# Performance work log

Hardware: AMD Instinct MI355X
Metric: run time of the kernel (lower is better)

## Reference

```python
import jax, jax.numpy as jnp
import numpy as np
from math import factorial

# ---- static config mirroring Cace.__init__ ----
MAX_L = 3            # max angular degree
N_RBF = 8            # Bessel radial basis size
RB = 8               # n_radial_basis (radial embedding dim after transform)
K = 3                # n_atom_basis -> edge channels C = K*K
NZ = 4               # len(zs)
CUTOFF = 5.5
N_NODES = 2000
N_EDGES = 50000
T_MP = 1             # num_message_passing
MP_NORM = 1.0 / np.sqrt(25.0)   # 1/sqrt(avg_num_neighbors)
C = K * K

def _lxlylz(max_l):
    out = []
    for l in range(max_l + 1):
        for lx in range(l, -1, -1):
            for ly in range(l - lx, -1, -1):
                out.append((lx, ly, l - lx - ly))
    return out

L_LIST = _lxlylz(MAX_L)                 # 20 Cartesian monomials for max_l=3
NL = len(L_LIST)
LX = np.array([t[0] for t in L_LIST]); LY = np.array([t[1] for t in L_LIST]); LZ = np.array([t[2] for t in L_LIST])
DEGS = LX + LY + LZ                     # degree l of each monomial
MULTI = np.array([factorial(int(d)) / (factorial(int(a)) * factorial(int(b)) * factorial(int(c)))
                  for a, b, c, d in zip(LX, LY, LZ, DEGS)], dtype=np.float32)
SEL = np.zeros((NL, MAX_L + 1), np.float32)
SEL[np.arange(NL), DEGS] = 1.0          # monomial -> degree one-hot (for per-l sums)
NB = 1 + (MAX_L + 1)                    # symmetrizer feats: nu=1 (l=0) + nu=2 per l

def bessel(r):  # [E] -> [E, N_RBF]
    n = jnp.arange(1, N_RBF + 1, dtype=r.dtype)
    return jnp.sqrt(2.0 / CUTOFF) * jnp.sin(n[None, :] * jnp.pi * r[:, None] / CUTOFF) / r[:, None]

def poly_cutoff(r):  # MACE-style polynomial cutoff, p=6
    p = 6.0
    u = r / CUTOFF
    f = 1.0 - (p + 1.0) * (p + 2.0) / 2.0 * u**6 + p * (p + 2.0) * u**7 - p * (p + 1.0) / 2.0 * u**8
    return f * (u < 1.0)

def axis_pows(x):  # [E] -> [E, MAX_L+1] = x^0..x^MAX_L (safe grads, handles negatives)
    pows = [jnp.ones_like(x)]
    for _ in range(MAX_L):
        pows.append(pows[-1] * x)
    return jnp.stack(pows, axis=1)

def angular(u):  # unit vectors [E,3] -> Cartesian monomials [E, NL]
    return axis_pows(u[:, 0])[:, LX] * axis_pows(u[:, 1])[:, LY] * axis_pows(u[:, 2])[:, LZ]

def radial_transform(x, W):  # x [N,R,L,C], W [MAX_L+1,R,Rb] shared per degree l
    return jnp.einsum('nrlc,lrb->nblc', x, W[DEGS])

def symmetrize(A):  # A [N,Rb,NL,C] -> B [N,Rb,NB,C]
    b1 = A[:, :, :1, :]  # nu=1: the (0,0,0) monomial (index 0)
    w = (A * A) * jnp.asarray(MULTI)[None, None, :, None]
    b2 = jnp.einsum('nrlc,lm->nrmc', w, jnp.asarray(SEL))  # nu=2 invariant per degree l
    return jnp.concatenate([b1, b2], axis=2)


def setup_inputs() -> dict:
    key = jax.random.key(0)
    ks = jax.random.split(key, 9)
    positions = jax.random.uniform(ks[0], (N_NODES, 3), dtype=jnp.float32) * 12.0
    species = jax.random.randint(ks[1], (N_NODES,), 0, NZ)
    send = jax.random.randint(ks[2], (N_EDGES,), 0, N_NODES)
    off = jax.random.randint(ks[3], (N_EDGES,), 1, N_NODES)
    recv = (send + off) % N_NODES  # no self-edges -> strictly positive edge lengths
    edge_index = jnp.stack([send, recv])
    shifts = jnp.zeros((N_EDGES, 3), jnp.float32)
    W_embed = jax.random.normal(ks[4], (NZ, K), jnp.float32)
    W_radial = jax.random.normal(ks[5], (MAX_L + 1, N_RBF, RB), jnp.float32) / np.sqrt(N_RBF)
    W_mem = jax.random.normal(ks[6], (MAX_L + 1, RB, RB), jnp.float32) / np.sqrt(RB)
    W_ar = jax.random.normal(ks[7], (N_RBF, RB), jnp.float32) / np.sqrt(N_RBF)
    W_chi = jax.random.normal(ks[8], (RB, NB), jnp.float32) * 0.1
    return {"positions": positions, "shifts": shifts, "W_embed": W_embed, "W_radial": W_radial,
            "W_mem": W_mem, "W_ar": W_ar, "W_chi": W_chi, "species": species, "edge_index": edge_index}


def reference(positions, shifts, W_embed, W_radial, W_mem, W_ar, W_chi, species, edge_index):
    n_nodes = positions.shape[0]
    send, recv = edge_index[0], edge_index[1]
    # edge geometry
    vec = positions[recv] - positions[send] + shifts
    lengths = jnp.linalg.norm(vec, axis=-1)
    u = vec / (lengths[:, None] + 1e-9)
    rad = bessel(lengths)          # [E,R]
    fcut = poly_cutoff(lengths)    # [E]
    ang = angular(u)               # [E,NL]
    # edge type encoding: outer product of sender/receiver species embeddings
    emb = W_embed[species]         # [N,K]
    enc = (emb[send][:, :, None] * emb[recv][:, None, :]).reshape(-1, C)  # [E,C]
    # elementwise_multiply_3tensors -> [E,R,NL,C]
    edge_attri = jnp.einsum('er,el,ec->erlc', rad * fcut[:, None], ang, enc)
    A = radial_transform(jax.ops.segment_sum(edge_attri, recv, num_segments=n_nodes), W_radial)  # [N,Rb,NL,C]
    B = symmetrize(A)              # [N,Rb,NB,C]
    feats = [B]
    for _ in range(T_MP):
        mem = jnp.einsum('nrlc,lrb->nblc', A, W_mem[DEGS])        # NodeMemory
        chi = jnp.einsum('nbkc,bk->nc', B, W_chi)                  # MessageBchi node scalar
        msg_bchi = edge_attri * chi[send][:, None, None, :]
        A_bchi = radial_transform(jax.ops.segment_sum(msg_bchi, recv, num_segments=n_nodes), W_radial)
        fr = (rad @ W_ar) * fcut[:, None]                          # MessageAr radial filter [E,Rb]
        msg_ar = A[send] * fr[:, :, None, None]
        A_ar = jax.ops.segment_sum(msg_ar, recv, num_segments=n_nodes)
        A = (A_ar + A_bchi) * MP_NORM + mem
        B = symmetrize(A)
        feats.append(B)
    return jnp.stack(feats, axis=-1)   # [N,Rb,NB,C,T_MP+1]
```

## Files before the change

### kernel.cpp

```cpp
#include <hip/hip_runtime.h>
#include <hip/hip_bf16.h>


#define CUTF 5.5f
#define MPNORM 0.2f

__constant__ int   d_DEGS[20]  = {0,1,1,1,2,2,2,2,2,2,3,3,3,3,3,3,3,3,3,3};
__constant__ float d_MULTI[20] = {1,1,1,1,1,2,2,1,2,1,1,3,3,3,6,3,1,3,3,1};

__global__ void k_count(const int* __restrict__ eidx, int* __restrict__ counts, int E) {
  int e = blockIdx.x * blockDim.x + threadIdx.x;
  if (e < E) atomicAdd(&counts[eidx[E + e]], 1);
}

__global__ void k_scan(const int* __restrict__ counts, int* __restrict__ offs, int N) {
  __shared__ int part[256];
  int t = threadIdx.x;
  int local[8]; int sum = 0;
  #pragma unroll
  for (int i = 0; i < 8; i++) {
    int idx = t*8 + i;
    int v = (idx < N) ? counts[idx] : 0;
    local[i] = sum; sum += v;
  }
  part[t] = sum; __syncthreads();
  for (int d = 1; d < 256; d <<= 1) {
    int add = (t >= d) ? part[t-d] : 0;
    __syncthreads();
    part[t] += add;
    __syncthreads();
  }
  int excl = part[t] - sum;
  #pragma unroll
  for (int i = 0; i < 8; i++) {
    int idx = t*8 + i;
    if (idx < N) offs[idx] = excl + local[i];
  }
  if (t == 255) offs[N] = part[255];
}

__global__ void k_edge(const float* __restrict__ pos,
                       const float* __restrict__ shifts,
                       const float* __restrict__ Wemb,
                       const float* __restrict__ War,
                       const int* __restrict__ species,
                       const int* __restrict__ eidx,
                       const int* __restrict__ offs,
                       int* __restrict__ cursor,
                       float* __restrict__ edata,
                       int* __restrict__ esend,
                       int E) {
  __shared__ float war_s[64];
  int t = threadIdx.x;
  if (t < 64) war_s[t] = War[t];
  __syncthreads();
  int e = blockIdx.x * blockDim.x + t;
  if (e >= E) return;
  int s  = eidx[e];
  int rI = eidx[E + e];
  float vx = pos[rI*3+0] - pos[s*3+0] + shifts[e*3+0];
  float vy = pos[rI*3+1] - pos[s*3+1] + shifts[e*3+1];
  float vz = pos[rI*3+2] - pos[s*3+2] + shifts[e*3+2];
  float len = sqrtf(vx*vx + vy*vy + vz*vz);
  float inv = 1.0f / (len + 1e-9f);
  float ux = vx*inv, uy = vy*inv, uz = vz*inv;
  float uu = len * (1.0f/CUTF);
  float u2 = uu*uu, u6 = u2*u2*u2;
  float fcut = (uu < 1.0f) ? (1.0f - 28.0f*u6 + 48.0f*u6*uu - 21.0f*u6*u2) : 0.0f;
  float x = 3.14159265358979f * uu;
  float sn = sinf(x), c2 = 2.0f*cosf(x), snm1 = 0.0f;
  float pref = sqrtf(2.0f/CUTF) / (len + 1e-20f);
  float rad[8];
  float v[48];
  #pragma unroll
  for (int k = 0; k < 8; k++) {
    rad[k] = pref * sn;
    v[k]   = rad[k] * fcut;
    float nxt = c2*sn - snm1; snm1 = sn; sn = nxt;
  }
  #pragma unroll
  for (int b = 0; b < 8; b++) {
    float a = 0.0f;
    #pragma unroll
    for (int k = 0; k < 8; k++) a += rad[k] * war_s[k*8+b];
    v[8+b] = a * fcut;
  }
  float px2 = ux*ux, py2 = uy*uy, pz2 = uz*uz;
  v[16] = 1.0f; v[17] = ux;     v[18] = uy;     v[19] = uz;
  v[20] = px2;  v[21] = ux*uy;  v[22] = ux*uz;  v[23] = py2;
  v[24] = uy*uz;v[25] = pz2;
  v[26] = px2*ux; v[27] = px2*uy; v[28] = px2*uz; v[29] = ux*py2;
  v[30] = ux*uy*uz; v[31] = ux*pz2; v[32] = py2*uy; v[33] = py2*uz;
  v[34] = uy*pz2; v[35] = pz2*uz;
  int zs = species[s], zr = species[rI];
  float es0 = Wemb[zs*3+0], es1 = Wemb[zs*3+1], es2 = Wemb[zs*3+2];
  float er0 = Wemb[zr*3+0], er1 = Wemb[zr*3+1], er2 = Wemb[zr*3+2];
  v[36] = es0*er0; v[37] = es0*er1; v[38] = es0*er2;
  v[39] = es1*er0; v[40] = es1*er1; v[41] = es1*er2;
  v[42] = es2*er0; v[43] = es2*er1; v[44] = es2*er2;
  v[45] = 0.0f; v[46] = 0.0f; v[47] = 0.0f;
  int slot = atomicAdd(&cursor[rI], 1);
  int dst = offs[rI] + slot;
  float4* eb4 = reinterpret_cast<float4*>(edata + (size_t)dst * 48);
  #pragma unroll
  for (int w = 0; w < 12; w++)
    eb4[w] = make_float4(v[4*w], v[4*w+1], v[4*w+2], v[4*w+3]);
  esend[dst] = s;
}

__global__ __launch_bounds__(192) void k_nodeA(
    const float* __restrict__ edata, const int* __restrict__ offs,
    const float* __restrict__ Wrad, const float* __restrict__ Wchi,
    float* __restrict__ A, unsigned int* __restrict__ Abf2,
    float* __restrict__ chi, float* __restrict__ B0, int N) {
  __shared__ float wr_s[288];
  __shared__ float wchi_s[40];
  __shared__ float Bsh[360];
  int t = threadIdx.x, n = blockIdx.x;
  for (int i = t; i < 256; i += 192) { int d = i >> 6, rm = i & 63; wr_s[d*72+rm] = Wrad[i]; }
  for (int i = t; i < 40;  i += 192) wchi_s[i] = Wchi[i];
  for (int i = t; i < 360; i += 192) Bsh[i] = 0.0f;
  int l = t / 9, c = t - l*9;
  bool act = t < 180;
  int ll = act ? l : 0, cc = act ? c : 0;
  float acc[8];
  #pragma unroll
  for (int r = 0; r < 8; r++) acc[r] = 0.0f;
  int start = offs[n], end = offs[n+1];
  #pragma unroll 4
  for (int j = start; j < end; j++) {
    const float* row = edata + (size_t)j * 48;
    float p = row[16+ll] * row[36+cc];
    #pragma unroll
    for (int r = 0; r < 8; r++) acc[r] += row[r] * p;
  }
  __syncthreads();
  int deg = act ? d_DEGS[ll] : 0;
  const float* wp = &wr_s[deg*72];
  float Ab[8];
  #pragma unroll
  for (int b = 0; b < 8; b++) {
    float a = 0.0f;
    #pragma unroll
    for (int r = 0; r < 8; r++) a += acc[r] * wp[r*8+b];
    Ab[b] = a;
  }
  if (act) {
    #pragma unroll
    for (int b = 0; b < 8; b++) A[(size_t)n*1440 + t*8 + b] = Ab[b];
    #pragma unroll
    for (int bp = 0; bp < 4; bp++) {
      __hip_bfloat16 blo = __float2bfloat16(Ab[2*bp]);
      __hip_bfloat16 bhi = __float2bfloat16(Ab[2*bp+1]);
      unsigned int pr = (unsigned int)(*reinterpret_cast<unsigned short*>(&blo))
                      | ((unsigned int)(*reinterpret_cast<unsigned short*>(&bhi)) << 16);
      Abf2[(size_t)bp*N*180 + (size_t)n*180 + t] = pr;
    }
    if (l == 0) {
      #pragma unroll
      for (int b = 0; b < 8; b++) Bsh[b*45 + c] = Ab[b];
    }
    float mlt = d_MULTI[ll]; int kk = 1 + deg;
    #pragma unroll
    for (int b = 0; b < 8; b++) atomicAdd(&Bsh[b*45 + kk*9 + c], mlt*Ab[b]*Ab[b]);
  }
  __syncthreads();
  if (t < 9) {
    float s = 0.0f;
    for (int b = 0; b < 8; b++)
      #pragma unroll
      for (int kq = 0; kq < 5; kq++) s += Bsh[b*45 + kq*9 + t] * wchi_s[b*5 + kq];
    chi[n*9 + t] = s;
  }
  for (int i = t; i < 360; i += 192)
    B0[(size_t)n*360 + i] = Bsh[i];
}

__global__ __launch_bounds__(192) void k_node2(
    const float* __restrict__ edata, const int* __restrict__ esend,
    const int* __restrict__ offs,
    const float* __restrict__ Wrad, const float* __restrict__ Wmem,
    const float* __restrict__ A, const unsigned int* __restrict__ Abf2,
    const float* __restrict__ chi, const float* __restrict__ B0,
    float* __restrict__ out, int N) {
  __shared__ float wr_s[288], wm_s[288];
  __shared__ float Bsh[360];
  int t = threadIdx.x, n = blockIdx.x;
  for (int i = t; i < 256; i += 192) {
    int d = i >> 6, rm = i & 63;
    wr_s[d*72+rm] = Wrad[i];
    wm_s[d*72+rm] = Wmem[i];
  }
  for (int i = t; i < 360; i += 192) Bsh[i] = 0.0f;
  int l = t / 9, c = t - l*9;
  bool act = t < 180;
  int ll = act ? l : 0, cc = act ? c : 0;
  int tt = act ? t : 0;
  size_t plane = (size_t)N * 180;
  float Sacc[8], ARacc[8];
  #pragma unroll
  for (int r = 0; r < 8; r++) { Sacc[r] = 0.0f; ARacc[r] = 0.0f; }
  int start = offs[n], end = offs[n+1];
  #pragma unroll 4
  for (int j = start; j < end; j++) {
    const float* row = edata + (size_t)j * 48;
    int snd = esend[j];
    float ch = chi[snd*9 + cc];
    float pch = row[16+ll] * row[36+cc] * ch;
    #pragma unroll
    for (int r = 0; r < 8; r++) Sacc[r] += row[r] * pch;
    const unsigned int* gp = Abf2 + (size_t)snd*180 + tt;
    unsigned int q0 = gp[0];
    unsigned int q1 = gp[plane];
    unsigned int q2 = gp[2*plane];
    unsigned int q3 = gp[3*plane];
    float a0 = __uint_as_float(q0 << 16), a1 = __uint_as_float(q0 & 0xffff0000u);
    float a2 = __uint_as_float(q1 << 16), a3 = __uint_as_float(q1 & 0xffff0000u);
    float a4 = __uint_as_float(q2 << 16), a5 = __uint_as_float(q2 & 0xffff0000u);
    float a6 = __uint_as_float(q3 << 16), a7 = __uint_as_float(q3 & 0xffff0000u);
    ARacc[0] += a0*row[8];  ARacc[1] += a1*row[9];
    ARacc[2] += a2*row[10]; ARacc[3] += a3*row[11];
    ARacc[4] += a4*row[12]; ARacc[5] += a5*row[13];
    ARacc[6] += a6*row[14]; ARacc[7] += a7*row[15];
  }
  __syncthreads();
  if (act) {
    int deg = d_DEGS[ll];
    const float* wrp = &wr_s[deg*72];
    const float* wmp = &wm_s[deg*72];
    const float* aop = A + (size_t)n*1440 + t*8;
    float aown[8];
    #pragma unroll
    for (int r = 0; r < 8; r++) aown[r] = aop[r];
    float newA[8];
    #pragma unroll
    for (int b = 0; b < 8; b++) {
      float mem = 0.0f, ab = 0.0f;
      #pragma unroll
      for (int r = 0; r < 8; r++) { mem += aown[r]*wmp[r*8+b]; ab += Sacc[r]*wrp[r*8+b]; }
      newA[b] = (ARacc[b] + ab)*MPNORM + mem;
    }
    if (l == 0) {
      #pragma unroll
      for (int b = 0; b < 8; b++) Bsh[b*45 + c] = newA[b];
    }
    float mlt = d_MULTI[ll]; int kk = 1 + deg;
    #pragma unroll
    for (int b = 0; b < 8; b++) atomicAdd(&Bsh[b*45 + kk*9 + c], mlt*newA[b]*newA[b]);
  }
  __syncthreads();
  float2* out2 = reinterpret_cast<float2*>(out);
  for (int i = t; i < 360; i += 192) {
    float2 pk; pk.x = B0[(size_t)n*360 + i]; pk.y = Bsh[i];
    out2[(size_t)n*360 + i] = pk;
  }
}

extern "C" void kernel_launch(void* const* d_in, const int* in_sizes, int n_in,
                              void* d_out, int out_size, void* d_ws, size_t ws_size,
                              hipStream_t stream) {
  const float* pos    = (const float*)d_in[0];
  const float* shifts = (const float*)d_in[1];
  const float* Wemb   = (const float*)d_in[2];
  const float* Wrad   = (const float*)d_in[3];
  const float* Wmem   = (const float*)d_in[4];
  const float* War    = (const float*)d_in[5];
  const float* Wchi   = (const float*)d_in[6];
  const int* species = (const int*)d_in[7];
  const int* eidx    = (const int*)d_in[8];
  float* out = (float*)d_out;
  int N = in_sizes[7];
  int E = in_sizes[8] / 2;

  char* base = (char*)d_ws;
  size_t off = 0;
  float* edata = (float*)(base + off); off += (size_t)E*48*4;
  float* A     = (float*)(base + off); off += (size_t)N*1440*4;
  unsigned int* Abf2 = (unsigned int*)(base + off); off += (size_t)N*180*4*4;
  float* chi   = (float*)(base + off); off += (size_t)N*9*4;
  float* B0    = (float*)(base + off); off += (size_t)N*360*4;
  int* counts  = (int*)(base + off);   off += (size_t)N*4;
  int* cursor  = (int*)(base + off);   off += (size_t)N*4;
  int* offs    = (int*)(base + off);   off += (((size_t)(N+1)*4) + 15) & ~(size_t)15;
  int* esend   = (int*)(base + off);   off += (size_t)E*4;

  hipMemsetAsync(counts, 0, (size_t)N*2*4, stream);
  int eb = (E + 255) / 256;
  k_count<<<eb, 256, 0, stream>>>(eidx, counts, E);
  k_scan<<<1, 256, 0, stream>>>(counts, offs, N);
  k_edge<<<eb, 256, 0, stream>>>(pos, shifts, Wemb, War, species, eidx, offs, cursor,
                                 edata, esend, E);
  k_nodeA<<<N, 192, 0, stream>>>(edata, offs, Wrad, Wchi, A, Abf2, chi, B0, N);
  k_node2<<<N, 192, 0, stream>>>(edata, esend, offs, Wrad, Wmem, A, Abf2, chi, B0, out, N);
}
```

Before: 169.2 us.

## Fuse count, scan and cursor reset into one kernel; interleave bf16 A gather

Replaces the memset, the global-atomic count kernel and the scan kernel with one 1024-thread block that histograms receivers in shared memory, scans them, and zeroes the cursor array. This removes two launches and a memset, but does all counting on a single workgroup. The bf16 copy of A also moves from four separate planes to one interleaved uint4 per (node, l, c), so each gather in k_node2 is a single 16-byte load instead of four scattered 4-byte loads. The shared histogram is limited to 2048 nodes.

```diff
diff --git a/kernel.cpp b/kernel.cpp
--- a/kernel.cpp
+++ b/kernel.cpp
@@ -8,35 +8,43 @@
 __constant__ int   d_DEGS[20]  = {0,1,1,1,2,2,2,2,2,2,3,3,3,3,3,3,3,3,3,3};
 __constant__ float d_MULTI[20] = {1,1,1,1,1,2,2,1,2,1,1,3,3,3,6,3,1,3,3,1};
 
-__global__ void k_count(const int* __restrict__ eidx, int* __restrict__ counts, int E) {
-  int e = blockIdx.x * blockDim.x + threadIdx.x;
-  if (e < E) atomicAdd(&counts[eidx[E + e]], 1);
-}
-
-__global__ void k_scan(const int* __restrict__ counts, int* __restrict__ offs, int N) {
-  __shared__ int part[256];
+__global__ __launch_bounds__(1024) void k_prep(const int* __restrict__ eidx,
+                                               int* __restrict__ offs,
+                                               int* __restrict__ cursor,
+                                               int N, int E) {
+  __shared__ int cnt[2048];
+  __shared__ int part[1024];
   int t = threadIdx.x;
-  int local[8]; int sum = 0;
-  #pragma unroll
-  for (int i = 0; i < 8; i++) {
-    int idx = t*8 + i;
-    int v = (idx < N) ? counts[idx] : 0;
-    local[i] = sum; sum += v;
-  }
-  part[t] = sum; __syncthreads();
-  for (int d = 1; d < 256; d <<= 1) {
-    int add = (t >= d) ? part[t-d] : 0;
+  cnt[t] = 0; cnt[t + 1024] = 0;
+  for (int i = t; i < N; i += 1024) cursor[i] = 0;
+  __syncthreads();
+  const int* recv = eidx + E;
+  if ((E & 3) == 0) {
+    #pragma unroll 2
+    for (int i = t * 4; i + 3 < E; i += 4096) {
+      int4 v = *reinterpret_cast<const int4*>(recv + i);
+      atomicAdd(&cnt[v.x], 1); atomicAdd(&cnt[v.y], 1);
+      atomicAdd(&cnt[v.z], 1); atomicAdd(&cnt[v.w], 1);
+    }
+  } else {
+    #pragma unroll 4
+    for (int i = t; i < E; i += 1024) atomicAdd(&cnt[recv[i]], 1);
+  }
+  __syncthreads();
+  int a = cnt[2 * t], b = cnt[2 * t + 1];
+  int s = a + b;
+  part[t] = s;
+  __syncthreads();
+  for (int d = 1; d < 1024; d <<= 1) {
+    int add = (t >= d) ? part[t - d] : 0;
     __syncthreads();
     part[t] += add;
     __syncthreads();
   }
-  int excl = part[t] - sum;
-  #pragma unroll
-  for (int i = 0; i < 8; i++) {
-    int idx = t*8 + i;
-    if (idx < N) offs[idx] = excl + local[i];
-  }
-  if (t == 255) offs[N] = part[255];
+  int excl = part[t] - s;
+  if (2 * t     < N) offs[2 * t]     = excl;
+  if (2 * t + 1 < N) offs[2 * t + 1] = excl + a;
+  if (t == 1023) offs[N] = part[1023];
 }
 
 __global__ void k_edge(const float* __restrict__ pos,
@@ -111,7 +119,7 @@
 __global__ __launch_bounds__(192) void k_nodeA(
     const float* __restrict__ edata, const int* __restrict__ offs,
     const float* __restrict__ Wrad, const float* __restrict__ Wchi,
-    float* __restrict__ A, unsigned int* __restrict__ Abf2,
+    float* __restrict__ A, uint4* __restrict__ Abf2,
     float* __restrict__ chi, float* __restrict__ B0, int N) {
   __shared__ float wr_s[288];
   __shared__ float wchi_s[40];
@@ -148,14 +156,16 @@
   if (act) {
     #pragma unroll
     for (int b = 0; b < 8; b++) A[(size_t)n*1440 + t*8 + b] = Ab[b];
+    unsigned int pk[4];
     #pragma unroll
     for (int bp = 0; bp < 4; bp++) {
       __hip_bfloat16 blo = __float2bfloat16(Ab[2*bp]);
       __hip_bfloat16 bhi = __float2bfloat16(Ab[2*bp+1]);
-      unsigned int pr = (unsigned int)(*reinterpret_cast<unsigned short*>(&blo))
-                      | ((unsigned int)(*reinterpret_cast<unsigned short*>(&bhi)) << 16);
-      Abf2[(size_t)bp*N*180 + (size_t)n*180 + t] = pr;
-    }
+      pk[bp] = (unsigned int)(*reinterpret_cast<unsigned short*>(&blo))
+             | ((unsigned int)(*reinterpret_cast<unsigned short*>(&bhi)) << 16);
+    }
+    uint4 q; q.x = pk[0]; q.y = pk[1]; q.z = pk[2]; q.w = pk[3];
+    Abf2[(size_t)n*180 + t] = q;
     if (l == 0) {
       #pragma unroll
       for (int b = 0; b < 8; b++) Bsh[b*45 + c] = Ab[b];
@@ -180,7 +190,7 @@
     const float* __restrict__ edata, const int* __restrict__ esend,
     const int* __restrict__ offs,
     const float* __restrict__ Wrad, const float* __restrict__ Wmem,
-    const float* __restrict__ A, const unsigned int* __restrict__ Abf2,
+    const float* __restrict__ A, const uint4* __restrict__ Abf2,
     const float* __restrict__ chi, const float* __restrict__ B0,
     float* __restrict__ out, int N) {
   __shared__ float wr_s[288], wm_s[288];
@@ -196,7 +206,6 @@
   bool act = t < 180;
   int ll = act ? l : 0, cc = act ? c : 0;
   int tt = act ? t : 0;
-  size_t plane = (size_t)N * 180;
   float Sacc[8], ARacc[8];
   #pragma unroll
   for (int r = 0; r < 8; r++) { Sacc[r] = 0.0f; ARacc[r] = 0.0f; }
@@ -209,15 +218,11 @@
     float pch = row[16+ll] * row[36+cc] * ch;
     #pragma unroll
     for (int r = 0; r < 8; r++) Sacc[r] += row[r] * pch;
-    const unsigned int* gp = Abf2 + (size_t)snd*180 + tt;
-    unsigned int q0 = gp[0];
-    unsigned int q1 = gp[plane];
-    unsigned int q2 = gp[2*plane];
-    unsigned int q3 = gp[3*plane];
-    float a0 = __uint_as_float(q0 << 16), a1 = __uint_as_float(q0 & 0xffff0000u);
-    float a2 = __uint_as_float(q1 << 16), a3 = __uint_as_float(q1 & 0xffff0000u);
-    float a4 = __uint_as_float(q2 << 16), a5 = __uint_as_float(q2 & 0xffff0000u);
-    float a6 = __uint_as_float(q3 << 16), a7 = __uint_as_float(q3 & 0xffff0000u);
+    const uint4 q = Abf2[(size_t)snd*180 + tt];
+    float a0 = __uint_as_float(q.x << 16), a1 = __uint_as_float(q.x & 0xffff0000u);
+    float a2 = __uint_as_float(q.y << 16), a3 = __uint_as_float(q.y & 0xffff0000u);
+    float a4 = __uint_as_float(q.z << 16), a5 = __uint_as_float(q.z & 0xffff0000u);
+    float a6 = __uint_as_float(q.w << 16), a7 = __uint_as_float(q.w & 0xffff0000u);
     ARacc[0] += a0*row[8];  ARacc[1] += a1*row[9];
     ARacc[2] += a2*row[10]; ARacc[3] += a3*row[11];
     ARacc[4] += a4*row[12]; ARacc[5] += a5*row[13];
@@ -276,18 +281,15 @@
   size_t off = 0;
   float* edata = (float*)(base + off); off += (size_t)E*48*4;
   float* A     = (float*)(base + off); off += (size_t)N*1440*4;
-  unsigned int* Abf2 = (unsigned int*)(base + off); off += (size_t)N*180*4*4;
+  uint4* Abf2  = (uint4*)(base + off); off += (size_t)N*180*16;
   float* chi   = (float*)(base + off); off += (size_t)N*9*4;
   float* B0    = (float*)(base + off); off += (size_t)N*360*4;
-  int* counts  = (int*)(base + off);   off += (size_t)N*4;
   int* cursor  = (int*)(base + off);   off += (size_t)N*4;
   int* offs    = (int*)(base + off);   off += (((size_t)(N+1)*4) + 15) & ~(size_t)15;
   int* esend   = (int*)(base + off);   off += (size_t)E*4;
 
-  hipMemsetAsync(counts, 0, (size_t)N*2*4, stream);
   int eb = (E + 255) / 256;
-  k_count<<<eb, 256, 0, stream>>>(eidx, counts, E);
-  k_scan<<<1, 256, 0, stream>>>(counts, offs, N);
+  k_prep<<<1, 1024, 0, stream>>>(eidx, offs, cursor, N, E);
   k_edge<<<eb, 256, 0, stream>>>(pos, shifts, Wemb, War, species, eidx, offs, cursor,
                                  edata, esend, E);
   k_nodeA<<<N, 192, 0, stream>>>(edata, offs, Wrad, Wchi, A, Abf2, chi, B0, N);
```

New measurement: 151.8 us. 10.2% less time.

## Record edge ranks in count pass, repack bf16 A gather into two uint2 planes

Applied to the files above, without the earlier changes.

The count kernel now saves each edge's atomic slot, so the edge kernel no longer needs a second atomic cursor, and one memset is dropped. The bf16 copy of A is repacked from four separate 32-bit planes into two 64-bit planes. The message-passing gather is split into two passes over the edges, each reading one plane with a vector load. This cuts the scattered neighbour loads per edge from four to two per pass. The cost is a second walk over the edge list and an extra erank buffer. The edge kernel also moves to 64-thread blocks.

```diff
diff --git a/kernel.cpp b/kernel.cpp
--- a/kernel.cpp
+++ b/kernel.cpp
@@ -8,9 +8,10 @@
 __constant__ int   d_DEGS[20]  = {0,1,1,1,2,2,2,2,2,2,3,3,3,3,3,3,3,3,3,3};
 __constant__ float d_MULTI[20] = {1,1,1,1,1,2,2,1,2,1,1,3,3,3,6,3,1,3,3,1};
 
-__global__ void k_count(const int* __restrict__ eidx, int* __restrict__ counts, int E) {
+__global__ void k_count(const int* __restrict__ eidx, int* __restrict__ counts,
+                        int* __restrict__ erank, int E) {
   int e = blockIdx.x * blockDim.x + threadIdx.x;
-  if (e < E) atomicAdd(&counts[eidx[E + e]], 1);
+  if (e < E) erank[e] = atomicAdd(&counts[eidx[E + e]], 1);
 }
 
 __global__ void k_scan(const int* __restrict__ counts, int* __restrict__ offs, int N) {
@@ -39,25 +40,27 @@
   if (t == 255) offs[N] = part[255];
 }
 
-__global__ void k_edge(const float* __restrict__ pos,
+__global__ __launch_bounds__(64) void k_edge(
+                       const float* __restrict__ pos,
                        const float* __restrict__ shifts,
                        const float* __restrict__ Wemb,
                        const float* __restrict__ War,
                        const int* __restrict__ species,
                        const int* __restrict__ eidx,
                        const int* __restrict__ offs,
-                       int* __restrict__ cursor,
+                       const int* __restrict__ erank,
                        float* __restrict__ edata,
                        int* __restrict__ esend,
                        int E) {
   __shared__ float war_s[64];
   int t = threadIdx.x;
-  if (t < 64) war_s[t] = War[t];
-  __syncthreads();
-  int e = blockIdx.x * blockDim.x + t;
+  war_s[t] = War[t];
+  __syncthreads();
+  int e = blockIdx.x * 64 + t;
   if (e >= E) return;
   int s  = eidx[e];
   int rI = eidx[E + e];
+  int rk = erank[e];
   float vx = pos[rI*3+0] - pos[s*3+0] + shifts[e*3+0];
   float vy = pos[rI*3+1] - pos[s*3+1] + shifts[e*3+1];
   float vz = pos[rI*3+2] - pos[s*3+2] + shifts[e*3+2];
@@ -99,8 +102,7 @@
   v[39] = es1*er0; v[40] = es1*er1; v[41] = es1*er2;
   v[42] = es2*er0; v[43] = es2*er1; v[44] = es2*er2;
   v[45] = 0.0f; v[46] = 0.0f; v[47] = 0.0f;
-  int slot = atomicAdd(&cursor[rI], 1);
-  int dst = offs[rI] + slot;
+  int dst = offs[rI] + rk;
   float4* eb4 = reinterpret_cast<float4*>(edata + (size_t)dst * 48);
   #pragma unroll
   for (int w = 0; w < 12; w++)
@@ -111,7 +113,7 @@
 __global__ __launch_bounds__(192) void k_nodeA(
     const float* __restrict__ edata, const int* __restrict__ offs,
     const float* __restrict__ Wrad, const float* __restrict__ Wchi,
-    float* __restrict__ A, unsigned int* __restrict__ Abf2,
+    float* __restrict__ A, uint2* __restrict__ Abf2lo, uint2* __restrict__ Abf2hi,
     float* __restrict__ chi, float* __restrict__ B0, int N) {
   __shared__ float wr_s[288];
   __shared__ float wchi_s[40];
@@ -148,14 +150,18 @@
   if (act) {
     #pragma unroll
     for (int b = 0; b < 8; b++) A[(size_t)n*1440 + t*8 + b] = Ab[b];
+    unsigned int pk[4];
     #pragma unroll
     for (int bp = 0; bp < 4; bp++) {
       __hip_bfloat16 blo = __float2bfloat16(Ab[2*bp]);
       __hip_bfloat16 bhi = __float2bfloat16(Ab[2*bp+1]);
-      unsigned int pr = (unsigned int)(*reinterpret_cast<unsigned short*>(&blo))
-                      | ((unsigned int)(*reinterpret_cast<unsigned short*>(&bhi)) << 16);
-      Abf2[(size_t)bp*N*180 + (size_t)n*180 + t] = pr;
+      pk[bp] = (unsigned int)(*reinterpret_cast<unsigned short*>(&blo))
+             | ((unsigned int)(*reinterpret_cast<unsigned short*>(&bhi)) << 16);
     }
+    uint2 qlo; qlo.x = pk[0]; qlo.y = pk[1];
+    uint2 qhi; qhi.x = pk[2]; qhi.y = pk[3];
+    Abf2lo[(size_t)n*180 + t] = qlo;
+    Abf2hi[(size_t)n*180 + t] = qhi;
     if (l == 0) {
       #pragma unroll
       for (int b = 0; b < 8; b++) Bsh[b*45 + c] = Ab[b];
@@ -180,7 +186,8 @@
     const float* __restrict__ edata, const int* __restrict__ esend,
     const int* __restrict__ offs,
     const float* __restrict__ Wrad, const float* __restrict__ Wmem,
-    const float* __restrict__ A, const unsigned int* __restrict__ Abf2,
+    const float* __restrict__ A,
+    const uint2* __restrict__ Abf2lo, const uint2* __restrict__ Abf2hi,
     const float* __restrict__ chi, const float* __restrict__ B0,
     float* __restrict__ out, int N) {
   __shared__ float wr_s[288], wm_s[288];
@@ -196,7 +203,6 @@
   bool act = t < 180;
   int ll = act ? l : 0, cc = act ? c : 0;
   int tt = act ? t : 0;
-  size_t plane = (size_t)N * 180;
   float Sacc[8], ARacc[8];
   #pragma unroll
   for (int r = 0; r < 8; r++) { Sacc[r] = 0.0f; ARacc[r] = 0.0f; }
@@ -206,20 +212,22 @@
     const float* row = edata + (size_t)j * 48;
     int snd = esend[j];
     float ch = chi[snd*9 + cc];
+    const uint2 ql = Abf2lo[(size_t)snd*180 + tt];
     float pch = row[16+ll] * row[36+cc] * ch;
     #pragma unroll
     for (int r = 0; r < 8; r++) Sacc[r] += row[r] * pch;
-    const unsigned int* gp = Abf2 + (size_t)snd*180 + tt;
-    unsigned int q0 = gp[0];
-    unsigned int q1 = gp[plane];
-    unsigned int q2 = gp[2*plane];
-    unsigned int q3 = gp[3*plane];
-    float a0 = __uint_as_float(q0 << 16), a1 = __uint_as_float(q0 & 0xffff0000u);
-    float a2 = __uint_as_float(q1 << 16), a3 = __uint_as_float(q1 & 0xffff0000u);
-    float a4 = __uint_as_float(q2 << 16), a5 = __uint_as_float(q2 & 0xffff0000u);
-    float a6 = __uint_as_float(q3 << 16), a7 = __uint_as_float(q3 & 0xffff0000u);
+    float a0 = __uint_as_float(ql.x << 16), a1 = __uint_as_float(ql.x & 0xffff0000u);
+    float a2 = __uint_as_float(ql.y << 16), a3 = __uint_as_float(ql.y & 0xffff0000u);
     ARacc[0] += a0*row[8];  ARacc[1] += a1*row[9];
     ARacc[2] += a2*row[10]; ARacc[3] += a3*row[11];
+  }
+  #pragma unroll 4
+  for (int j = start; j < end; j++) {
+    const float* row = edata + (size_t)j * 48;
+    int snd = esend[j];
+    const uint2 qh = Abf2hi[(size_t)snd*180 + tt];
+    float a4 = __uint_as_float(qh.x << 16), a5 = __uint_as_float(qh.x & 0xffff0000u);
+    float a6 = __uint_as_float(qh.y << 16), a7 = __uint_as_float(qh.y & 0xffff0000u);
     ARacc[4] += a4*row[12]; ARacc[5] += a5*row[13];
     ARacc[6] += a6*row[14]; ARacc[7] += a7*row[15];
   }
@@ -276,20 +284,21 @@
   size_t off = 0;
   float* edata = (float*)(base + off); off += (size_t)E*48*4;
   float* A     = (float*)(base + off); off += (size_t)N*1440*4;
-  unsigned int* Abf2 = (unsigned int*)(base + off); off += (size_t)N*180*4*4;
+  uint2* Abf2lo = (uint2*)(base + off); off += (size_t)N*180*8;
+  uint2* Abf2hi = (uint2*)(base + off); off += (size_t)N*180*8;
   float* chi   = (float*)(base + off); off += (size_t)N*9*4;
   float* B0    = (float*)(base + off); off += (size_t)N*360*4;
   int* counts  = (int*)(base + off);   off += (size_t)N*4;
-  int* cursor  = (int*)(base + off);   off += (size_t)N*4;
   int* offs    = (int*)(base + off);   off += (((size_t)(N+1)*4) + 15) & ~(size_t)15;
   int* esend   = (int*)(base + off);   off += (size_t)E*4;
-
-  hipMemsetAsync(counts, 0, (size_t)N*2*4, stream);
-  int eb = (E + 255) / 256;
-  k_count<<<eb, 256, 0, stream>>>(eidx, counts, E);
+  int* erank   = (int*)(base + off);   off += (((size_t)E*4) + 15) & ~(size_t)15;
+
+  hipMemsetAsync(counts, 0, (size_t)N*4, stream);
+  k_count<<<(E + 255) / 256, 256, 0, stream>>>(eidx, counts, erank, E);
   k_scan<<<1, 256, 0, stream>>>(counts, offs, N);
-  k_edge<<<eb, 256, 0, stream>>>(pos, shifts, Wemb, War, species, eidx, offs, cursor,
-                                 edata, esend, E);
-  k_nodeA<<<N, 192, 0, stream>>>(edata, offs, Wrad, Wchi, A, Abf2, chi, B0, N);
-  k_node2<<<N, 192, 0, stream>>>(edata, esend, offs, Wrad, Wmem, A, Abf2, chi, B0, out, N);
-}
+  k_edge<<<(E + 63) / 64, 64, 0, stream>>>(pos, shifts, Wemb, War, species, eidx,
+                                           offs, erank, edata, esend, E);
+  k_nodeA<<<N, 192, 0, stream>>>(edata, offs, Wrad, Wchi, A, Abf2lo, Abf2hi, chi, B0, N);
+  k_node2<<<N, 192, 0, stream>>>(edata, esend, offs, Wrad, Wmem, A, Abf2lo, Abf2hi,
+                                 chi, B0, out, N);
+}
```

After: 158.3 us. -6.4%, faster.
